# Kernel optimization log

Measured on AMD Instinct MI355X. Metric: run time of the kernel, lower is better.

The kernel has to match this reference:

```python
import jax, jax.numpy as jnp
import numpy as np

LATENT, CTX, HID, TDIM, HEADS = 512, 512, 1024, 128, 8
HEAD_DIM = HID // HEADS
SCALE = HEAD_DIM ** -0.5


def _ln(x, g, b, eps=1e-5):
    m = jnp.mean(x, axis=-1, keepdims=True)
    v = jnp.mean((x - m) ** 2, axis=-1, keepdims=True)
    return (x - m) * jax.lax.rsqrt(v + eps) * g + b


def _time_embed(t):
    half = TDIM // 2
    exponent = jnp.linspace(0.0, 1.0, half, dtype=t.dtype)
    freqs = jnp.exp(jnp.log(1000.0) * exponent)
    ang = 2.0 * jnp.pi * t[:, None] * freqs[None, :]
    return jnp.concatenate([jnp.sin(ang), jnp.cos(ang)], axis=-1)  # [B, TDIM]


def setup_inputs() -> dict:
    key = jax.random.key(0)
    ks = iter(jax.random.split(key, 32))
    B, M = 4096, 64

    def w(k, i, o):
        return jax.random.normal(k, (i, o), jnp.float32) * 0.02

    inp = {
        "states": jax.random.normal(next(ks), (B, LATENT), jnp.float32),
        "time_values": jax.random.uniform(next(ks), (B,), jnp.float32),
        "class_summary": jax.random.normal(next(ks), (B, CTX), jnp.float32),
        "support_memory": jax.random.normal(next(ks), (B, M, LATENT), jnp.float32),
        # state_trunk: LN(latent+tdim) -> Linear -> GELU -> Linear
        "trunk_ln_g": jnp.ones((LATENT + TDIM,)), "trunk_ln_b": jnp.zeros((LATENT + TDIM,)),
        "trunk_w1": w(next(ks), LATENT + TDIM, HID), "trunk_b1": jnp.zeros((HID,)),
        "trunk_w2": w(next(ks), HID, HID), "trunk_b2": jnp.zeros((HID,)),
        # memory adapter: LN(latent) -> Linear(latent, hid)
        "mem_ln_g": jnp.ones((LATENT,)), "mem_ln_b": jnp.zeros((LATENT,)),
        "mem_w": w(next(ks), LATENT, HID), "mem_b": jnp.zeros((HID,)),
        # attention projections
        "wq": w(next(ks), HID, HID), "bq": jnp.zeros((HID,)),
        "wk": w(next(ks), HID, HID), "bk": jnp.zeros((HID,)),
        "wv": w(next(ks), HID, HID), "bv": jnp.zeros((HID,)),
        "wo": w(next(ks), HID, HID), "bo": jnp.zeros((HID,)),
        # pre-condition norm + FiLM
        "pre_ln_g": jnp.ones((HID,)), "pre_ln_b": jnp.zeros((HID,)),
        "film_w": w(next(ks), CTX, 2 * HID), "film_b": jnp.zeros((2 * HID,)),
        # conditioner: LN -> Linear -> GELU -> Linear
        "cond_ln_g": jnp.ones((HID,)), "cond_ln_b": jnp.zeros((HID,)),
        "cond_w1": w(next(ks), HID, HID), "cond_b1": jnp.zeros((HID,)),
        "cond_w2": w(next(ks), HID, HID), "cond_b2": jnp.zeros((HID,)),
        # output head: LN -> Linear -> GELU -> Linear(hid, latent)
        "head_ln_g": jnp.ones((HID,)), "head_ln_b": jnp.zeros((HID,)),
        "head_w1": w(next(ks), HID, HID), "head_b1": jnp.zeros((HID,)),
        "head_w2": w(next(ks), HID, LATENT), "head_b2": jnp.zeros((LATENT,)),
    }
    return inp


def _forward(states, time_values, class_summary, support_memory,
             trunk_ln_g, trunk_ln_b, trunk_w1, trunk_b1, trunk_w2, trunk_b2,
             mem_ln_g, mem_ln_b, mem_w, mem_b,
             wq, bq, wk, bk, wv, bv, wo, bo,
             pre_ln_g, pre_ln_b, film_w, film_b,
             cond_ln_g, cond_ln_b, cond_w1, cond_b1, cond_w2, cond_b2,
             head_ln_g, head_ln_b, head_w1, head_b1, head_w2, head_b2):
    B, M, _ = support_memory.shape
    gelu = lambda x: jax.nn.gelu(x, approximate=False)

    # trunk: g = Trunk([y, gamma(t)])
    te = _time_embed(time_values)
    x = _ln(jnp.concatenate([states, te], axis=-1), trunk_ln_g, trunk_ln_b)
    g = gelu(x @ trunk_w1 + trunk_b1) @ trunk_w2 + trunk_b2  # [B, HID]

    # encode memory + single-query multi-head attention
    mem_h = _ln(support_memory, mem_ln_g, mem_ln_b) @ mem_w + mem_b  # [B, M, HID]
    q = (g @ wq + bq).reshape(B, HEADS, HEAD_DIM)
    k = (mem_h @ wk + bk).reshape(B, M, HEADS, HEAD_DIM)
    v = (mem_h @ wv + bv).reshape(B, M, HEADS, HEAD_DIM)
    logits = jnp.einsum("bhd,bmhd->bhm", q, k) * SCALE
    attn = jax.nn.softmax(logits, axis=-1)
    summary = jnp.einsum("bhm,bmhd->bhd", attn, v).reshape(B, HID)
    attn_summary = summary @ wo + bo

    # FiLM conditioning
    combined = _ln(g + attn_summary, pre_ln_g, pre_ln_b)
    film = class_summary @ film_w + film_b
    scale, shift = film[:, :HID], film[:, HID:]
    combined = (1.0 + scale) * combined + shift
    cond_x = _ln(combined, cond_ln_g, cond_ln_b)
    conditioned = gelu(cond_x @ cond_w1 + cond_b1) @ cond_w2 + cond_b2 + combined

    # output head
    hx = _ln(conditioned, head_ln_g, head_ln_b)
    return gelu(hx @ head_w1 + head_b1) @ head_w2 + head_b2  # [B, LATENT]


def reference(states, time_values, class_summary, support_memory,
              trunk_ln_g, trunk_ln_b, trunk_w1, trunk_b1, trunk_w2, trunk_b2,
              mem_ln_g, mem_ln_b, mem_w, mem_b,
              wq, bq, wk, bk, wv, bv, wo, bo,
              pre_ln_g, pre_ln_b, film_w, film_b,
              cond_ln_g, cond_ln_b, cond_w1, cond_b1, cond_w2, cond_b2,
              head_ln_g, head_ln_b, head_w1, head_b1, head_w2, head_b2):
    return _forward(states, time_values, class_summary, support_memory,
                    trunk_ln_g, trunk_ln_b, trunk_w1, trunk_b1, trunk_w2, trunk_b2,
                    mem_ln_g, mem_ln_b, mem_w, mem_b,
                    wq, bq, wk, bk, wv, bv, wo, bo,
                    pre_ln_g, pre_ln_b, film_w, film_b,
                    cond_ln_g, cond_ln_b, cond_w1, cond_b1, cond_w2, cond_b2,
                    head_ln_g, head_ln_b, head_w1, head_b1, head_w2, head_b2)
```

## Files before the change

kernel.cpp:

```cpp
#include <hip/hip_runtime.h>
#include <cstdint>
#include <cstddef>

typedef unsigned short ushort_t;
typedef short s16x8 __attribute__((ext_vector_type(8)));
typedef float f32x4 __attribute__((ext_vector_type(4)));

__device__ __forceinline__ float bf2f(ushort_t h){
  union { unsigned int u; float f; } v; v.u = ((unsigned int)h) << 16; return v.f;
}
__device__ __forceinline__ ushort_t f2bf(float x){
  union { float f; unsigned int u; } v; v.f = x;
  unsigned int r = v.u + 0x7FFFu + ((v.u >> 16) & 1u);
  return (ushort_t)(r >> 16);
}
__device__ __forceinline__ float gelu_f(float x){
  return 0.5f * x * (1.0f + erff(x * 0.7071067811865475f));
}
__device__ __forceinline__ float wave_sum(float v){
  #pragma unroll
  for (int o = 32; o; o >>= 1) v += __shfl_xor(v, o);
  return v;
}
__device__ __forceinline__ void block_reduce2(float& s, float& q, float* red){
  s = wave_sum(s); q = wave_sum(q);
  int w = threadIdx.x >> 6, lane = threadIdx.x & 63, nw = blockDim.x >> 6;
  if (lane == 0){ red[w] = s; red[8 + w] = q; }
  __syncthreads();
  float ts = 0.f, tq = 0.f;
  for (int i = 0; i < nw; ++i){ ts += red[i]; tq += red[8 + i]; }
  __syncthreads();
  s = ts; q = tq;
}

struct TDesc { const float* in; ushort_t* out; int K; int N; int start; };
struct PrepArgs {
  TDesc t[11];
  int ntiles_end;
  int cast1_blocks;
  int cast_end;
  const float* memw; ushort_t* memwb;
  const float* csum; ushort_t* csb;
  const float* memb; const float* wv; const float* bvp; float* bv2;
};

__global__ __launch_bounds__(256) void prep_k(PrepArgs a){
  int bid = blockIdx.x, tid = threadIdx.x;
  if (bid < a.ntiles_end){
    int d = 0;
    #pragma unroll
    for (int i = 1; i < 11; ++i) if (bid >= a.t[i].start) d = i;
    TDesc td = a.t[d];
    int tile = bid - td.start;
    int tilesx = td.N >> 5;
    int n0 = (tile % tilesx) << 5, k0 = (tile / tilesx) << 5;
    __shared__ float tbuf[32][33];
    int tx = tid & 31, ty = tid >> 5;
    #pragma unroll
    for (int j = 0; j < 32; j += 8)
      tbuf[ty + j][tx] = td.in[(size_t)(k0 + ty + j) * td.N + (n0 + tx)];
    __syncthreads();
    #pragma unroll
    for (int j = 0; j < 32; j += 8)
      td.out[(size_t)(n0 + ty + j) * td.K + (k0 + tx)] = f2bf(tbuf[tx][ty + j]);
  } else if (bid < a.cast_end){
    int ci = bid - a.ntiles_end;
    const float* src; ushort_t* dst; int i;
    if (ci < a.cast1_blocks){ src = a.memw; dst = a.memwb; i = ci * 1024 + tid * 4; }
    else { src = a.csum; dst = a.csb; i = (ci - a.cast1_blocks) * 1024 + tid * 4; }
    float4 v = *(const float4*)(src + i);
    union { ushort_t u[4]; uint2 p; } pk;
    pk.u[0] = f2bf(v.x); pk.u[1] = f2bf(v.y); pk.u[2] = f2bf(v.z); pk.u[3] = f2bf(v.w);
    *(uint2*)(dst + i) = pk.p;
  } else {
    int col = (bid - a.cast_end) * 256 + tid;
    float a0 = 0.f, a1 = 0.f, a2 = 0.f, a3 = 0.f;
    for (int j = 0; j < 1024; j += 4){
      a0 += a.memb[j + 0] * a.wv[(size_t)(j + 0) * 1024 + col];
      a1 += a.memb[j + 1] * a.wv[(size_t)(j + 1) * 1024 + col];
      a2 += a.memb[j + 2] * a.wv[(size_t)(j + 2) * 1024 + col];
      a3 += a.memb[j + 3] * a.wv[(size_t)(j + 3) * 1024 + col];
    }
    a.bv2[col] = a0 + a1 + a2 + a3 + a.bvp[col];
  }
}

__global__ __launch_bounds__(256) void ln_trunk_k(const float* __restrict__ states, const float* __restrict__ tv,
    const float* __restrict__ g, const float* __restrict__ b, ushort_t* __restrict__ out){
  int row = blockIdx.x, tid = threadIdx.x;
  __shared__ float buf[640];
  __shared__ float red[16];
  float t = tv[row];
  for (int i = tid; i < 640; i += 256){
    float v;
    if (i < 512) v = states[(size_t)row * 512 + i];
    else {
      int j = i - 512, jj = j & 63;
      float fr = expf(6.907755278982137f * ((float)jj * (1.0f / 63.0f)));
      float ang = 6.283185307179586f * t * fr;
      v = (j < 64) ? sinf(ang) : cosf(ang);
    }
    buf[i] = v;
  }
  __syncthreads();
  float s = 0.f, q = 0.f;
  for (int i = tid; i < 640; i += 256){ float v = buf[i]; s += v; q += v * v; }
  block_reduce2(s, q, red);
  float mean = s * (1.0f / 640.0f);
  float var = q * (1.0f / 640.0f) - mean * mean;
  float rstd = rsqrtf(var + 1e-5f);
  for (int i = tid; i < 640; i += 256)
    out[(size_t)row * 640 + i] = f2bf((buf[i] - mean) * rstd * g[i] + b[i]);
}

__global__ __launch_bounds__(256) void ln_rows_k(const float* __restrict__ in, const float* __restrict__ g,
    const float* __restrict__ b, ushort_t* __restrict__ out, int D){
  int row = blockIdx.x, tid = threadIdx.x, i = tid * 4;
  __shared__ float red[16];
  const float* x = in + (size_t)row * D;
  float4 v = *(const float4*)(x + i);
  float s = v.x + v.y + v.z + v.w;
  float q = v.x * v.x + v.y * v.y + v.z * v.z + v.w * v.w;
  block_reduce2(s, q, red);
  float invD = 1.0f / (float)D;
  float mean = s * invD, var = q * invD - mean * mean, rstd = rsqrtf(var + 1e-5f);
  union { ushort_t u[4]; uint2 p; } pk;
  pk.u[0] = f2bf((v.x - mean) * rstd * g[i + 0] + b[i + 0]);
  pk.u[1] = f2bf((v.y - mean) * rstd * g[i + 1] + b[i + 1]);
  pk.u[2] = f2bf((v.z - mean) * rstd * g[i + 2] + b[i + 2]);
  pk.u[3] = f2bf((v.w - mean) * rstd * g[i + 3] + b[i + 3]);
  *(uint2*)(out + (size_t)row * D + i) = pk.p;
}

__global__ __launch_bounds__(256) void fuse_film_k(const float* __restrict__ gf, const float* __restrict__ asf,
    const float* __restrict__ film, const float* __restrict__ pg, const float* __restrict__ pb,
    const float* __restrict__ cg, const float* __restrict__ cb,
    float* __restrict__ c2f, ushort_t* __restrict__ cxb){
  int row = blockIdx.x, tid = threadIdx.x, i = tid * 4;
  __shared__ float red[16];
  float4 a = *(const float4*)(gf + (size_t)row * 1024 + i);
  float4 d = *(const float4*)(asf + (size_t)row * 1024 + i);
  float x[4] = { a.x + d.x, a.y + d.y, a.z + d.z, a.w + d.w };
  float s = x[0] + x[1] + x[2] + x[3];
  float q = x[0]*x[0] + x[1]*x[1] + x[2]*x[2] + x[3]*x[3];
  block_reduce2(s, q, red);
  float mean = s * (1.0f / 1024.0f), var = q * (1.0f / 1024.0f) - mean * mean;
  float rstd = rsqrtf(var + 1e-5f);
  float4 pgv = *(const float4*)(pg + i), pbv = *(const float4*)(pb + i);
  float4 sc = *(const float4*)(film + (size_t)row * 2048 + i);
  float4 sh = *(const float4*)(film + (size_t)row * 2048 + 1024 + i);
  float c2[4];
  {
    float pgx[4] = { pgv.x, pgv.y, pgv.z, pgv.w };
    float pbx[4] = { pbv.x, pbv.y, pbv.z, pbv.w };
    float scx[4] = { sc.x, sc.y, sc.z, sc.w };
    float shx[4] = { sh.x, sh.y, sh.z, sh.w };
    #pragma unroll
    for (int e = 0; e < 4; ++e){
      float cc = (x[e] - mean) * rstd * pgx[e] + pbx[e];
      c2[e] = (1.0f + scx[e]) * cc + shx[e];
    }
  }
  *(float4*)(c2f + (size_t)row * 1024 + i) = make_float4(c2[0], c2[1], c2[2], c2[3]);
  float s2 = c2[0] + c2[1] + c2[2] + c2[3];
  float q2 = c2[0]*c2[0] + c2[1]*c2[1] + c2[2]*c2[2] + c2[3]*c2[3];
  block_reduce2(s2, q2, red);
  float m2 = s2 * (1.0f / 1024.0f), v2 = q2 * (1.0f / 1024.0f) - m2 * m2;
  float r2 = rsqrtf(v2 + 1e-5f);
  float4 cgv = *(const float4*)(cg + i), cbv = *(const float4*)(cb + i);
  union { ushort_t u[4]; uint2 p; } pk;
  pk.u[0] = f2bf((c2[0] - m2) * r2 * cgv.x + cbv.x);
  pk.u[1] = f2bf((c2[1] - m2) * r2 * cgv.y + cbv.y);
  pk.u[2] = f2bf((c2[2] - m2) * r2 * cgv.z + cbv.z);
  pk.u[3] = f2bf((c2[3] - m2) * r2 * cgv.w + cbv.w);
  *(uint2*)(cxb + (size_t)row * 1024 + i) = pk.p;
}

__global__ __launch_bounds__(256, 2) void suppattn_k(
    const float* __restrict__ support, const float* __restrict__ lgw, const float* __restrict__ lbw,
    const ushort_t* __restrict__ U, ushort_t* __restrict__ R)
{
  __shared__ ushort_t S[64 * 512];
  __shared__ ushort_t UG[9 * 512];
  __shared__ float WT[8][64];
  __shared__ float SUMV[64], SUMSQ[64];
  __shared__ __align__(16) float MEANR[64];
  __shared__ __align__(16) float RSTDR[64];
  __shared__ float PMAX[4][8], PSUM[4][8], PMU[4][8];
  __shared__ float AB[2][8];
  __shared__ float MUH[8];

  int bb = blockIdx.x, tid = threadIdx.x, w = tid >> 6, l = tid & 63;
  const ushort_t* Ub = U + (size_t)bb * 4096;

  for (int id = tid; id < 576; id += 256){
    int hr = id >> 6, cc = id & 63;
    int byteoff = hr * 1024 + (((cc & 56) | ((cc & 7) ^ (hr & 7))) << 4);
    uint4* dst = (uint4*)((char*)UG + byteoff);
    if (hr < 8){
      s16x8 uv = *(const s16x8*)(Ub + hr * 512 + cc * 8);
      float4 g0 = *(const float4*)(lgw + cc * 8);
      float4 g1 = *(const float4*)(lgw + cc * 8 + 4);
      float ga[8] = { g0.x, g0.y, g0.z, g0.w, g1.x, g1.y, g1.z, g1.w };
      union { ushort_t u[8]; uint4 p; } pk;
      #pragma unroll
      for (int e = 0; e < 8; ++e) pk.u[e] = f2bf(ga[e] * bf2f((ushort_t)uv[e]));
      *dst = pk.p;
    } else {
      *dst = make_uint4(0x3F803F80u, 0x3F803F80u, 0x3F803F80u, 0x3F803F80u);
    }
  }

  {
    int h0 = 2 * w, h1 = 2 * w + 1;
    s16x8 u0 = *(const s16x8*)(Ub + h0 * 512 + l * 8);
    s16x8 u1 = *(const s16x8*)(Ub + h1 * 512 + l * 8);
    float4 g0 = *(const float4*)(lgw + l * 8), g1 = *(const float4*)(lgw + l * 8 + 4);
    float4 c0 = *(const float4*)(lbw + l * 8), c1 = *(const float4*)(lbw + l * 8 + 4);
    float ga[8] = { g0.x, g0.y, g0.z, g0.w, g1.x, g1.y, g1.z, g1.w };
    float ba[8] = { c0.x, c0.y, c0.z, c0.w, c1.x, c1.y, c1.z, c1.w };
    float A0 = 0.f, B0 = 0.f, A1 = 0.f, B1 = 0.f;
    #pragma unroll
    for (int e = 0; e < 8; ++e){
      float x0 = bf2f((ushort_t)u0[e]), x1 = bf2f((ushort_t)u1[e]);
      A0 += ba[e] * x0; B0 += ga[e] * x0;
      A1 += ba[e] * x1; B1 += ga[e] * x1;
    }
    A0 = wave_sum(A0); B0 = wave_sum(B0); A1 = wave_sum(A1); B1 = wave_sum(B1);
    if (l == 0){ AB[0][h0] = A0; AB[1][h0] = B0; AB[0][h1] = A1; AB[1][h1] = B1; }
  }

  #pragma unroll 4
  for (int i = 0; i < 16; ++i){
    int m = i * 4 + w;
    const float* row = support + ((size_t)bb * 64 + m) * 512 + l * 8;
    float4 a0 = *(const float4*)row, a1 = *(const float4*)(row + 4);
    union { ushort_t u[8]; uint4 p; } pk;
    pk.u[0] = f2bf(a0.x); pk.u[1] = f2bf(a0.y); pk.u[2] = f2bf(a0.z); pk.u[3] = f2bf(a0.w);
    pk.u[4] = f2bf(a1.x); pk.u[5] = f2bf(a1.y); pk.u[6] = f2bf(a1.z); pk.u[7] = f2bf(a1.w);
    int byteoff = m * 1024 + (((l & 56) | ((l & 7) ^ (m & 7))) << 4);
    *(uint4*)((char*)S + byteoff) = pk.p;
  }
  __syncthreads();

  int l15 = l & 15, lk = l >> 4;
  int hr = (l15 < 8) ? l15 : 8;
  int arowb = (w * 16 + l15) * 1024;
  int hrowb = hr * 1024;
  f32x4 dacc = (f32x4){0.f, 0.f, 0.f, 0.f};
  f32x4 sacc = (f32x4){0.f, 0.f, 0.f, 0.f};
  #pragma unroll
  for (int ks = 0; ks < 16; ++ks){
    int cc = ks * 4 + lk;
    s16x8 afr = *(const s16x8*)((char*)S + arowb + (((cc & 56) | ((cc & 7) ^ (l15 & 7))) << 4));
    s16x8 bfr = *(const s16x8*)((char*)UG + hrowb + (((cc & 56) | ((cc & 7) ^ (hr & 7))) << 4));
    dacc = __builtin_amdgcn_mfma_f32_16x16x32_bf16(afr, bfr, dacc, 0, 0, 0);
    sacc = __builtin_amdgcn_mfma_f32_16x16x32_bf16(afr, afr, sacc, 0, 0, 0);
  }
  if (l15 == 8){
    #pragma unroll
    for (int j = 0; j < 4; ++j) SUMV[w * 16 + lk * 4 + j] = dacc[j];
  }
  if ((l15 >> 2) == lk) SUMSQ[w * 16 + l15] = sacc[l15 & 3];
  __syncthreads();
  if (tid < 64){
    float mean = SUMV[tid] * (1.0f / 512.0f);
    float var = SUMSQ[tid] * (1.0f / 512.0f) - mean * mean;
    MEANR[tid] = mean;
    RSTDR[tid] = rsqrtf(var + 1e-5f);
  }
  __syncthreads();

  int r0 = w * 16 + lk * 4;
  float4 mns = *(const float4*)(MEANR + r0);
  float4 rst = *(const float4*)(RSTDR + r0);
  float mn[4] = { mns.x, mns.y, mns.z, mns.w };
  float rs[4] = { rst.x, rst.y, rst.z, rst.w };
  float Ah = AB[0][l15 & 7], Bh = AB[1][l15 & 7];
  float lg[4];
  #pragma unroll
  for (int j = 0; j < 4; ++j)
    lg[j] = 0.08838834764831845f * (rs[j] * (dacc[j] - mn[j] * Bh) + Ah);
  float lmax = fmaxf(fmaxf(lg[0], lg[1]), fmaxf(lg[2], lg[3]));
  lmax = fmaxf(lmax, __shfl_xor(lmax, 16));
  lmax = fmaxf(lmax, __shfl_xor(lmax, 32));
  if (l < 8) PMAX[w][l] = lmax;
  __syncthreads();
  float gmax = fmaxf(fmaxf(PMAX[0][l15 & 7], PMAX[1][l15 & 7]),
                     fmaxf(PMAX[2][l15 & 7], PMAX[3][l15 & 7]));
  float e4[4]; float ls = 0.f, lm = 0.f;
  #pragma unroll
  for (int j = 0; j < 4; ++j){
    e4[j] = __expf(lg[j] - gmax);
    ls += e4[j];
    lm += e4[j] * rs[j] * mn[j];
  }
  ls += __shfl_xor(ls, 16); ls += __shfl_xor(ls, 32);
  lm += __shfl_xor(lm, 16); lm += __shfl_xor(lm, 32);
  if (l < 8){ PSUM[w][l] = ls; PMU[w][l] = lm; }
  __syncthreads();
  float Sh = PSUM[0][l15 & 7] + PSUM[1][l15 & 7] + PSUM[2][l15 & 7] + PSUM[3][l15 & 7];
  float inv = 1.0f / Sh;
  if (l15 < 8){
    #pragma unroll
    for (int j = 0; j < 4; ++j) WT[l15][r0 + j] = e4[j] * rs[j] * inv;
  }
  if (w == 0 && l < 8){
    MUH[l] = (PMU[0][l] + PMU[1][l] + PMU[2][l] + PMU[3][l]) * inv;
  }
  __syncthreads();

  int h0 = 2 * w, h1 = 2 * w + 1;
  float acc0[8] = {0.f,0.f,0.f,0.f,0.f,0.f,0.f,0.f};
  float acc1[8] = {0.f,0.f,0.f,0.f,0.f,0.f,0.f,0.f};
  #pragma unroll 4
  for (int m = 0; m < 64; ++m){
    s16x8 sv = *(const s16x8*)((char*)S + m * 1024 + (((l & 56) | ((l & 7) ^ (m & 7))) << 4));
    float f0 = WT[h0][m], f1 = WT[h1][m];
    #pragma unroll
    for (int e = 0; e < 8; ++e){
      float x = bf2f((ushort_t)sv[e]);
      acc0[e] += f0 * x;
      acc1[e] += f1 * x;
    }
  }
  {
    float4 g0 = *(const float4*)(lgw + l * 8), g1 = *(const float4*)(lgw + l * 8 + 4);
    float4 c0 = *(const float4*)(lbw + l * 8), c1 = *(const float4*)(lbw + l * 8 + 4);
    float ga[8] = { g0.x, g0.y, g0.z, g0.w, g1.x, g1.y, g1.z, g1.w };
    float ba[8] = { c0.x, c0.y, c0.z, c0.w, c1.x, c1.y, c1.z, c1.w };
    float mu0 = MUH[h0], mu1 = MUH[h1];
    union { ushort_t u[8]; uint4 p; } p0, p1;
    #pragma unroll
    for (int e = 0; e < 8; ++e){
      p0.u[e] = f2bf(ga[e] * (acc0[e] - mu0) + ba[e]);
      p1.u[e] = f2bf(ga[e] * (acc1[e] - mu1) + ba[e]);
    }
    *(uint4*)(R + (size_t)bb * 4096 + h0 * 512 + l * 8) = p0.p;
    *(uint4*)(R + (size_t)bb * 4096 + h1 * 512 + l * 8) = p1.p;
  }
}

#define GLL16(gsrc, ldst) \
  __builtin_amdgcn_global_load_lds((const __attribute__((address_space(1))) unsigned int*)(gsrc), \
                                   (__attribute__((address_space(3))) unsigned int*)(ldst), 16, 0, 0)

template<bool GELU, bool BIAS, bool WF32, bool WBF16, bool RESID>
__global__ __launch_bounds__(256, 3) void gemm_k(
    const ushort_t* __restrict__ A, int lda, long long aZ,
    const ushort_t* __restrict__ Bt, int ldb, long long bZ,
    const float* __restrict__ bias, long long biasZ,
    float* __restrict__ C, int ldc, long long cZ,
    ushort_t* __restrict__ Cb, int ldcb, long long cbZ,
    const float* __restrict__ R, int ldr,
    int M, int N, int K)
{
  __shared__ ushort_t smA[2][64 * 64];
  __shared__ ushort_t smB[2][128 * 64];
  int tid = threadIdx.x, lane = tid & 63, w = tid >> 6;
  int z = blockIdx.z;
  A  += (size_t)aZ * z;
  Bt += (size_t)bZ * z;
  if (BIAS)  bias += (size_t)biasZ * z;
  if (WF32)  C    += (size_t)cZ * z;
  if (WBF16) Cb   += (size_t)cbZ * z;
  int m0 = blockIdx.y * 64, n0 = blockIdx.x * 128;
  int nk = K >> 6;

  auto stage = [&](int buf, int kt){
    int k0 = kt << 6;
    #pragma unroll
    for (int i = 0; i < 2; ++i){
      int c = ((w << 1) + i) * 64 + lane;
      int rowl = c >> 3, sp = c & 7;
      int sg = sp ^ (rowl & 7);
      GLL16(A + (size_t)(m0 + rowl) * lda + (k0 + sg * 8), &smA[buf][((w << 1) + i) * 512]);
    }
    #pragma unroll
    for (int i = 0; i < 4; ++i){
      int c = ((w << 2) + i) * 64 + lane;
      int rowl = c >> 3, sp = c & 7;
      int sg = sp ^ (rowl & 7);
      GLL16(Bt + (size_t)(n0 + rowl) * ldb + (k0 + sg * 8), &smB[buf][((w << 2) + i) * 512]);
    }
  };

  int qrow = w >> 1, qcol = w & 1;
  int l15 = lane & 15, lk = lane >> 4, l7 = lane & 7;
  int sb0 = ((0 + lk) ^ l7) << 4;
  int sb1 = ((4 + lk) ^ l7) << 4;
  int arow = (qrow * 32 + l15) * 128;
  int brow = (qcol * 64 + l15) * 128;

  f32x4 acc[2][4];
  #pragma unroll
  for (int m = 0; m < 2; ++m)
    #pragma unroll
    for (int n = 0; n < 4; ++n)
      acc[m][n] = (f32x4){0.f, 0.f, 0.f, 0.f};

  stage(0, 0);
  asm volatile("s_waitcnt vmcnt(0)" ::: "memory");
  __syncthreads();
  for (int kt = 0; kt < nk; ++kt){
    int cur = kt & 1;
    if (kt + 1 < nk) stage((kt + 1) & 1, kt + 1);
    const char* ab = (const char*)&smA[cur][0];
    const char* bbp = (const char*)&smB[cur][0];
    s16x8 af[2][2], bfv[4][2];
    #pragma unroll
    for (int m = 0; m < 2; ++m){
      af[m][0] = *(const s16x8*)(ab + arow + m * 2048 + sb0);
      af[m][1] = *(const s16x8*)(ab + arow + m * 2048 + sb1);
    }
    #pragma unroll
    for (int n = 0; n < 4; ++n){
      bfv[n][0] = *(const s16x8*)(bbp + brow + n * 2048 + sb0);
      bfv[n][1] = *(const s16x8*)(bbp + brow + n * 2048 + sb1);
    }
    #pragma unroll
    for (int kb = 0; kb < 2; ++kb)
      #pragma unroll
      for (int m = 0; m < 2; ++m)
        #pragma unroll
        for (int n = 0; n < 4; ++n)
          acc[m][n] = __builtin_amdgcn_mfma_f32_16x16x32_bf16(af[m][kb], bfv[n][kb], acc[m][n], 0, 0, 0);
    asm volatile("s_waitcnt vmcnt(0)" ::: "memory");
    __syncthreads();
  }

  #pragma unroll
  for (int n = 0; n < 4; ++n){
    int col = n0 + qcol * 64 + n * 16 + l15;
    float bvv = BIAS ? bias[col] : 0.0f;
    #pragma unroll
    for (int m = 0; m < 2; ++m){
      int rbase = m0 + qrow * 32 + m * 16 + lk * 4;
      #pragma unroll
      for (int r = 0; r < 4; ++r){
        float x = acc[m][n][r] + bvv;
        if (GELU) x = gelu_f(x);
        int row = rbase + r;
        if (RESID) x += R[(size_t)row * ldr + col];
        if (WF32)  C[(size_t)row * ldc + col] = x;
        if (WBF16) Cb[(size_t)row * ldcb + col] = f2bf(x);
      }
    }
  }
}

extern "C" void kernel_launch(void* const* d_in, const int* in_sizes, int n_in,
                              void* d_out, int out_size, void* d_ws, size_t ws_size,
                              hipStream_t stream)
{
  (void)in_sizes; (void)n_in; (void)out_size;
  const float* states      = (const float*)d_in[0];
  const float* time_values = (const float*)d_in[1];
  const float* class_sum   = (const float*)d_in[2];
  const float* support     = (const float*)d_in[3];
  const float* trunk_ln_g  = (const float*)d_in[4];
  const float* trunk_ln_b  = (const float*)d_in[5];
  const float* trunk_w1    = (const float*)d_in[6];
  const float* trunk_b1    = (const float*)d_in[7];
  const float* trunk_w2    = (const float*)d_in[8];
  const float* trunk_b2    = (const float*)d_in[9];
  const float* mem_ln_g    = (const float*)d_in[10];
  const float* mem_ln_b    = (const float*)d_in[11];
  const float* mem_w       = (const float*)d_in[12];
  const float* mem_b       = (const float*)d_in[13];
  const float* wq          = (const float*)d_in[14];
  const float* bq          = (const float*)d_in[15];
  const float* wk          = (const float*)d_in[16];
  const float* wv          = (const float*)d_in[18];
  const float* bvp         = (const float*)d_in[19];
  const float* wo          = (const float*)d_in[20];
  const float* bo          = (const float*)d_in[21];
  const float* pre_g       = (const float*)d_in[22];
  const float* pre_b       = (const float*)d_in[23];
  const float* film_w      = (const float*)d_in[24];
  const float* film_b      = (const float*)d_in[25];
  const float* cond_g      = (const float*)d_in[26];
  const float* cond_b      = (const float*)d_in[27];
  const float* cond_w1     = (const float*)d_in[28];
  const float* cond_b1     = (const float*)d_in[29];
  const float* cond_w2     = (const float*)d_in[30];
  const float* cond_b2     = (const float*)d_in[31];
  const float* head_g      = (const float*)d_in[32];
  const float* head_bb     = (const float*)d_in[33];
  const float* head_w1     = (const float*)d_in[34];
  const float* head_b1     = (const float*)d_in[35];
  const float* head_w2     = (const float*)d_in[36];
  const float* head_b2     = (const float*)d_in[37];
  float* out = (float*)d_out;

  char* ws = (char*)d_ws;
  size_t off = 0;
  auto alloc = [&](size_t bytes)->char*{
    char* p = ws + off;
    off += (bytes + 255) & ~(size_t)255;
    return p;
  };
  ushort_t* tw1T   = (ushort_t*)alloc((size_t)640 * 1024 * 2);
  ushort_t* tw2T   = (ushort_t*)alloc((size_t)1024 * 1024 * 2);
  ushort_t* wqT    = (ushort_t*)alloc((size_t)1024 * 1024 * 2);
  ushort_t* wkT    = (ushort_t*)alloc((size_t)1024 * 1024 * 2);
  ushort_t* wvT    = (ushort_t*)alloc((size_t)1024 * 1024 * 2);
  ushort_t* woT    = (ushort_t*)alloc((size_t)1024 * 1024 * 2);
  ushort_t* memw_b = (ushort_t*)alloc((size_t)512 * 1024 * 2);
  ushort_t* filmWT = (ushort_t*)alloc((size_t)512 * 2048 * 2);
  ushort_t* cw1T   = (ushort_t*)alloc((size_t)1024 * 1024 * 2);
  ushort_t* cw2T   = (ushort_t*)alloc((size_t)1024 * 1024 * 2);
  ushort_t* hw1T   = (ushort_t*)alloc((size_t)1024 * 1024 * 2);
  ushort_t* hw2T   = (ushort_t*)alloc((size_t)1024 * 512 * 2);
  ushort_t* K2     = (ushort_t*)alloc((size_t)512 * 1024 * 2);
  ushort_t* V2T    = (ushort_t*)alloc((size_t)1024 * 512 * 2);
  float*    bv2    = (float*)   alloc((size_t)1024 * 4);
  ushort_t* xnb    = (ushort_t*)alloc((size_t)4096 * 640 * 2);
  ushort_t* h1     = (ushort_t*)alloc((size_t)4096 * 1024 * 2);
  float*    gf     = (float*)   alloc((size_t)4096 * 1024 * 4);
  ushort_t* gb     = (ushort_t*)alloc((size_t)4096 * 1024 * 2);
  ushort_t* qb     = (ushort_t*)alloc((size_t)4096 * 1024 * 2);
  ushort_t* U      = (ushort_t*)alloc((size_t)4096 * 4096 * 2);
  ushort_t* Rb     = (ushort_t*)alloc((size_t)4096 * 4096 * 2);
  ushort_t* sumb   = (ushort_t*)alloc((size_t)4096 * 1024 * 2);
  float*    asf    = (float*)   alloc((size_t)4096 * 1024 * 4);
  ushort_t* csb    = (ushort_t*)alloc((size_t)4096 * 512 * 2);
  float*    filmf  = (float*)   alloc((size_t)4096 * 2048 * 4);
  float*    c2f    = (float*)   alloc((size_t)4096 * 1024 * 4);
  ushort_t* cxb    = (ushort_t*)alloc((size_t)4096 * 1024 * 2);
  ushort_t* c1     = (ushort_t*)alloc((size_t)4096 * 1024 * 2);
  float*    cond2f = (float*)   alloc((size_t)4096 * 1024 * 4);
  ushort_t* hxb    = (ushort_t*)alloc((size_t)4096 * 1024 * 2);
  ushort_t* h3     = (ushort_t*)alloc((size_t)4096 * 1024 * 2);
  if (off > ws_size) return;

  PrepArgs pa;
  int s = 0;
  auto setT = [&](int i, const float* in, ushort_t* o, int K, int N){
    pa.t[i].in = in; pa.t[i].out = o; pa.t[i].K = K; pa.t[i].N = N; pa.t[i].start = s;
    s += (N >> 5) * (K >> 5);
  };
  setT(0, trunk_w1, tw1T, 640, 1024);
  setT(1, trunk_w2, tw2T, 1024, 1024);
  setT(2, wq, wqT, 1024, 1024);
  setT(3, wk, wkT, 1024, 1024);
  setT(4, wv, wvT, 1024, 1024);
  setT(5, wo, woT, 1024, 1024);
  setT(6, film_w, filmWT, 512, 2048);
  setT(7, cond_w1, cw1T, 1024, 1024);
  setT(8, cond_w2, cw2T, 1024, 1024);
  setT(9, head_w1, hw1T, 1024, 1024);
  setT(10, head_w2, hw2T, 1024, 512);
  pa.ntiles_end = s;
  pa.cast1_blocks = (512 * 1024) / 1024;
  pa.cast_end = s + pa.cast1_blocks + (4096 * 512) / 1024;
  pa.memw = mem_w; pa.memwb = memw_b;
  pa.csum = class_sum; pa.csb = csb;
  pa.memb = mem_b; pa.wv = wv; pa.bvp = bvp; pa.bv2 = bv2;
  prep_k<<<pa.cast_end + 4, 256, 0, stream>>>(pa);

  gemm_k<false, false, false, true, false><<<dim3(8, 8, 1), 256, 0, stream>>>(
      memw_b, 1024, 0, wkT, 1024, 0, nullptr, 0, nullptr, 0, 0, K2, 1024, 0, nullptr, 0, 512, 1024, 1024);
  gemm_k<false, false, false, true, false><<<dim3(4, 16, 1), 256, 0, stream>>>(
      wvT, 1024, 0, memw_b, 1024, 0, nullptr, 0, nullptr, 0, 0, V2T, 512, 0, nullptr, 0, 1024, 512, 1024);

  ln_trunk_k<<<4096, 256, 0, stream>>>(states, time_values, trunk_ln_g, trunk_ln_b, xnb);
  gemm_k<true, true, false, true, false><<<dim3(8, 64, 1), 256, 0, stream>>>(
      xnb, 640, 0, tw1T, 640, 0, trunk_b1, 0, nullptr, 0, 0, h1, 1024, 0, nullptr, 0, 4096, 1024, 640);
  gemm_k<false, true, true, true, false><<<dim3(8, 64, 1), 256, 0, stream>>>(
      h1, 1024, 0, tw2T, 1024, 0, trunk_b2, 0, gf, 1024, 0, gb, 1024, 0, nullptr, 0, 4096, 1024, 1024);
  gemm_k<false, true, false, true, false><<<dim3(8, 64, 1), 256, 0, stream>>>(
      gb, 1024, 0, wqT, 1024, 0, bq, 0, nullptr, 0, 0, qb, 1024, 0, nullptr, 0, 4096, 1024, 1024);
  gemm_k<false, false, false, true, false><<<dim3(4, 64, 8), 256, 0, stream>>>(
      qb, 1024, 128, K2, 1024, 128, nullptr, 0, nullptr, 0, 0, U, 4096, 512, nullptr, 0, 4096, 512, 128);

  suppattn_k<<<4096, 256, 0, stream>>>(support, mem_ln_g, mem_ln_b, U, Rb);

  gemm_k<false, true, false, true, false><<<dim3(1, 64, 8), 256, 0, stream>>>(
      Rb, 4096, 512, V2T, 512, 65536, bv2, 128, nullptr, 0, 0, sumb, 1024, 128, nullptr, 0, 4096, 128, 512);

  gemm_k<false, true, true, false, false><<<dim3(8, 64, 1), 256, 0, stream>>>(
      sumb, 1024, 0, woT, 1024, 0, bo, 0, asf, 1024, 0, nullptr, 0, 0, nullptr, 0, 4096, 1024, 1024);
  gemm_k<false, true, true, false, false><<<dim3(16, 64, 1), 256, 0, stream>>>(
      csb, 512, 0, filmWT, 512, 0, film_b, 0, filmf, 2048, 0, nullptr, 0, 0, nullptr, 0, 4096, 2048, 512);

  fuse_film_k<<<4096, 256, 0, stream>>>(gf, asf, filmf, pre_g, pre_b, cond_g, cond_b, c2f, cxb);

  gemm_k<true, true, false, true, false><<<dim3(8, 64, 1), 256, 0, stream>>>(
      cxb, 1024, 0, cw1T, 1024, 0, cond_b1, 0, nullptr, 0, 0, c1, 1024, 0, nullptr, 0, 4096, 1024, 1024);
  gemm_k<false, true, true, false, true><<<dim3(8, 64, 1), 256, 0, stream>>>(
      c1, 1024, 0, cw2T, 1024, 0, cond_b2, 0, cond2f, 1024, 0, nullptr, 0, 0, c2f, 1024, 4096, 1024, 1024);
  ln_rows_k<<<4096, 256, 0, stream>>>(cond2f, head_g, head_bb, hxb, 1024);
  gemm_k<true, true, false, true, false><<<dim3(8, 64, 1), 256, 0, stream>>>(
      hxb, 1024, 0, hw1T, 1024, 0, head_b1, 0, nullptr, 0, 0, h3, 1024, 0, nullptr, 0, 4096, 1024, 1024);
  gemm_k<false, true, true, false, false><<<dim3(4, 64, 1), 256, 0, stream>>>(
      h3, 1024, 0, hw2T, 1024, 0, head_b2, 0, out, 512, 0, nullptr, 0, 0, nullptr, 0, 4096, 512, 1024);
}
```

Baseline: 481.7 us.

## Triple-buffer GEMM LDS pipeline, fuse residual add into Wo GEMM, store FiLM as bf16

The GEMM kernel moves from double to triple buffering in LDS, prefetching two k-tiles ahead with a partial vmcnt wait so global loads overlap more compute. Launch bounds drop from 3 to 2 blocks per CU to fit the extra shared memory. The Wo projection now adds the trunk output as a residual in its epilogue, which removes one fp32 read in the FiLM fuse kernel. The FiLM scale and shift are written and read as bf16 instead of fp32, halving that traffic at the cost of some precision.

```diff
diff --git a/kernel.cpp b/kernel.cpp
--- a/kernel.cpp
+++ b/kernel.cpp
@@ -132,33 +132,31 @@
   *(uint2*)(out + (size_t)row * D + i) = pk.p;
 }
 
-__global__ __launch_bounds__(256) void fuse_film_k(const float* __restrict__ gf, const float* __restrict__ asf,
-    const float* __restrict__ film, const float* __restrict__ pg, const float* __restrict__ pb,
+__global__ __launch_bounds__(256) void fuse_film_k(const float* __restrict__ combf, const ushort_t* __restrict__ filmb,
+    const float* __restrict__ pg, const float* __restrict__ pb,
     const float* __restrict__ cg, const float* __restrict__ cb,
     float* __restrict__ c2f, ushort_t* __restrict__ cxb){
   int row = blockIdx.x, tid = threadIdx.x, i = tid * 4;
   __shared__ float red[16];
-  float4 a = *(const float4*)(gf + (size_t)row * 1024 + i);
-  float4 d = *(const float4*)(asf + (size_t)row * 1024 + i);
-  float x[4] = { a.x + d.x, a.y + d.y, a.z + d.z, a.w + d.w };
+  float4 a = *(const float4*)(combf + (size_t)row * 1024 + i);
+  float x[4] = { a.x, a.y, a.z, a.w };
   float s = x[0] + x[1] + x[2] + x[3];
   float q = x[0]*x[0] + x[1]*x[1] + x[2]*x[2] + x[3]*x[3];
   block_reduce2(s, q, red);
   float mean = s * (1.0f / 1024.0f), var = q * (1.0f / 1024.0f) - mean * mean;
   float rstd = rsqrtf(var + 1e-5f);
   float4 pgv = *(const float4*)(pg + i), pbv = *(const float4*)(pb + i);
-  float4 sc = *(const float4*)(film + (size_t)row * 2048 + i);
-  float4 sh = *(const float4*)(film + (size_t)row * 2048 + 1024 + i);
+  union { uint2 p; ushort_t u[4]; } scv, shv;
+  scv.p = *(const uint2*)(filmb + (size_t)row * 2048 + i);
+  shv.p = *(const uint2*)(filmb + (size_t)row * 2048 + 1024 + i);
   float c2[4];
   {
     float pgx[4] = { pgv.x, pgv.y, pgv.z, pgv.w };
     float pbx[4] = { pbv.x, pbv.y, pbv.z, pbv.w };
-    float scx[4] = { sc.x, sc.y, sc.z, sc.w };
-    float shx[4] = { sh.x, sh.y, sh.z, sh.w };
     #pragma unroll
     for (int e = 0; e < 4; ++e){
       float cc = (x[e] - mean) * rstd * pgx[e] + pbx[e];
-      c2[e] = (1.0f + scx[e]) * cc + shx[e];
+      c2[e] = (1.0f + bf2f(scv.u[e])) * cc + bf2f(shv.u[e]);
     }
   }
   *(float4*)(c2f + (size_t)row * 1024 + i) = make_float4(c2[0], c2[1], c2[2], c2[3]);
@@ -346,7 +344,7 @@
                                    (__attribute__((address_space(3))) unsigned int*)(ldst), 16, 0, 0)
 
 template<bool GELU, bool BIAS, bool WF32, bool WBF16, bool RESID>
-__global__ __launch_bounds__(256, 3) void gemm_k(
+__global__ __launch_bounds__(256, 2) void gemm_k(
     const ushort_t* __restrict__ A, int lda, long long aZ,
     const ushort_t* __restrict__ Bt, int ldb, long long bZ,
     const float* __restrict__ bias, long long biasZ,
@@ -355,8 +353,8 @@
     const float* __restrict__ R, int ldr,
     int M, int N, int K)
 {
-  __shared__ ushort_t smA[2][64 * 64];
-  __shared__ ushort_t smB[2][128 * 64];
+  __shared__ ushort_t smA[3][64 * 64];
+  __shared__ ushort_t smB[3][128 * 64];
   int tid = threadIdx.x, lane = tid & 63, w = tid >> 6;
   int z = blockIdx.z;
   A  += (size_t)aZ * z;
@@ -400,11 +398,17 @@
       acc[m][n] = (f32x4){0.f, 0.f, 0.f, 0.f};
 
   stage(0, 0);
-  asm volatile("s_waitcnt vmcnt(0)" ::: "memory");
-  __syncthreads();
+  if (nk > 1){
+    stage(1, 1);
+    asm volatile("s_waitcnt vmcnt(6)" ::: "memory");
+  } else {
+    asm volatile("s_waitcnt vmcnt(0)" ::: "memory");
+  }
+  __syncthreads();
+
+  int cur = 0, st = 2;
   for (int kt = 0; kt < nk; ++kt){
-    int cur = kt & 1;
-    if (kt + 1 < nk) stage((kt + 1) & 1, kt + 1);
+    if (kt + 2 < nk) stage(st, kt + 2);
     const char* ab = (const char*)&smA[cur][0];
     const char* bbp = (const char*)&smB[cur][0];
     s16x8 af[2][2], bfv[4][2];
@@ -425,8 +429,15 @@
         #pragma unroll
         for (int n = 0; n < 4; ++n)
           acc[m][n] = __builtin_amdgcn_mfma_f32_16x16x32_bf16(af[m][kb], bfv[n][kb], acc[m][n], 0, 0, 0);
-    asm volatile("s_waitcnt vmcnt(0)" ::: "memory");
-    __syncthreads();
+    if (kt + 2 < nk){
+      asm volatile("s_waitcnt vmcnt(6)" ::: "memory");
+      __syncthreads();
+    } else if (kt + 1 < nk){
+      asm volatile("s_waitcnt vmcnt(0)" ::: "memory");
+      __syncthreads();
+    }
+    cur = (cur == 2) ? 0 : cur + 1;
+    st  = (st  == 2) ? 0 : st  + 1;
   }
 
   #pragma unroll
@@ -523,9 +534,9 @@
   ushort_t* U      = (ushort_t*)alloc((size_t)4096 * 4096 * 2);
   ushort_t* Rb     = (ushort_t*)alloc((size_t)4096 * 4096 * 2);
   ushort_t* sumb   = (ushort_t*)alloc((size_t)4096 * 1024 * 2);
-  float*    asf    = (float*)   alloc((size_t)4096 * 1024 * 4);
+  float*    combf  = (float*)   alloc((size_t)4096 * 1024 * 4);
   ushort_t* csb    = (ushort_t*)alloc((size_t)4096 * 512 * 2);
-  float*    filmf  = (float*)   alloc((size_t)4096 * 2048 * 4);
+  ushort_t* filmb  = (ushort_t*)alloc((size_t)4096 * 2048 * 2);
   float*    c2f    = (float*)   alloc((size_t)4096 * 1024 * 4);
   ushort_t* cxb    = (ushort_t*)alloc((size_t)4096 * 1024 * 2);
   ushort_t* c1     = (ushort_t*)alloc((size_t)4096 * 1024 * 2);
@@ -579,12 +590,12 @@
   gemm_k<false, true, false, true, false><<<dim3(1, 64, 8), 256, 0, stream>>>(
       Rb, 4096, 512, V2T, 512, 65536, bv2, 128, nullptr, 0, 0, sumb, 1024, 128, nullptr, 0, 4096, 128, 512);
 
-  gemm_k<false, true, true, false, false><<<dim3(8, 64, 1), 256, 0, stream>>>(
-      sumb, 1024, 0, woT, 1024, 0, bo, 0, asf, 1024, 0, nullptr, 0, 0, nullptr, 0, 4096, 1024, 1024);
-  gemm_k<false, true, true, false, false><<<dim3(16, 64, 1), 256, 0, stream>>>(
-      csb, 512, 0, filmWT, 512, 0, film_b, 0, filmf, 2048, 0, nullptr, 0, 0, nullptr, 0, 4096, 2048, 512);
-
-  fuse_film_k<<<4096, 256, 0, stream>>>(gf, asf, filmf, pre_g, pre_b, cond_g, cond_b, c2f, cxb);
+  gemm_k<false, true, true, false, true><<<dim3(8, 64, 1), 256, 0, stream>>>(
+      sumb, 1024, 0, woT, 1024, 0, bo, 0, combf, 1024, 0, nullptr, 0, 0, gf, 1024, 4096, 1024, 1024);
+  gemm_k<false, true, false, true, false><<<dim3(16, 64, 1), 256, 0, stream>>>(
+      csb, 512, 0, filmWT, 512, 0, film_b, 0, nullptr, 0, 0, filmb, 2048, 0, nullptr, 0, 4096, 2048, 512);
+
+  fuse_film_k<<<4096, 256, 0, stream>>>(combf, filmb, pre_g, pre_b, cond_g, cond_b, c2f, cxb);
 
   gemm_k<true, true, false, true, false><<<dim3(8, 64, 1), 256, 0, stream>>>(
       cxb, 1024, 0, cw1T, 1024, 0, cond_b1, 0, nullptr, 0, 0, c1, 1024, 0, nullptr, 0, 4096, 1024, 1024);
```

Result: no change. 484.3 us (+0.5%).
